# Optimization experiments

Hardware: AMD Instinct MI355X
Metric: run time of the kernel (lower is better)

Reference implementation:

```python
import jax, jax.numpy as jnp
import numpy as np

B, C, H, W = 16, 512, 32, 32

def _conv2d(x, w, b, pad):
    y = jax.lax.conv_general_dilated(
        x, w, window_strides=(1, 1), padding=[(pad, pad), (pad, pad)],
        dimension_numbers=('NCHW', 'OIHW', 'NCHW'))
    return y + b[None, :, None, None]

def setup_inputs() -> dict:
    key = jax.random.key(0)
    ks = jax.random.split(key, 10)
    s3 = 1.0 / np.sqrt(C * 9)   # torch conv2d default init scale (3x3)
    s1 = 1.0 / np.sqrt(3 * C)   # 1x1 conv over 3C input channels
    return {
        'x':  jax.random.normal(ks[0], (B, C, H, W), jnp.float32),
        'w1': jax.random.uniform(ks[1], (C, C, 3, 3), jnp.float32, -s3, s3),
        'b1': jax.random.uniform(ks[2], (C,), jnp.float32, -s3, s3),
        'w2': jax.random.uniform(ks[3], (C, C, 3, 3), jnp.float32, -s3, s3),
        'b2': jax.random.uniform(ks[4], (C,), jnp.float32, -s3, s3),
        'w3': jax.random.uniform(ks[5], (C, C, 3, 3), jnp.float32, -s3, s3),
        'b3': jax.random.uniform(ks[6], (C,), jnp.float32, -s3, s3),
        'alpha': jax.random.normal(ks[7], (), jnp.float32) * 0.1,
        'beta':  jax.random.normal(ks[8], (), jnp.float32) * 0.1,
        'wf': jax.random.uniform(ks[9], (C, 3 * C, 1, 1), jnp.float32, -s1, s1),
        'bf': jnp.zeros((C,), jnp.float32),
    }

def reference(x, w1, b1, w2, b2, w3, b3, alpha, beta, wf, bf):
    b, c, h, w = x.shape
    n = h * w
    # --- spatial attention ---
    A = _conv2d(x, w1, b1, 1).reshape(b, c, n)  # [b,C,N]
    Bm = _conv2d(x, w2, b2, 1).reshape(b, c, n)
    D = _conv2d(x, w3, b3, 1).reshape(b, c, n)
    M = jnp.einsum('bcn,bcm->bnm', A, Bm)       # A^T @ B, [b,N,N]
    M = jax.nn.softmax(M, axis=-1)
    # weighted_C = M @ D^T -> [b,N,C]; then permute to [b,C,N]
    spat = jnp.einsum('bnm,bcm->bcn', M, D).reshape(b, c, h, w)
    spat = alpha * spat
    # --- channel attention ---
    Xr = x.reshape(b, c, n)                     # [b,C,N]
    S = jnp.einsum('bcn,bdn->bcd', Xr, Xr)      # [b,C,C]
    S = jax.nn.softmax(S, axis=-1)
    # weighted = S^T @ Xr
    chan = jnp.einsum('bdc,bdn->bcn', S, Xr).reshape(b, c, h, w)
    chan = beta * chan
    # --- fuse ---
    cat = jnp.concatenate((x, spat, chan), axis=1)  # [b,3C,H,W]
    return _conv2d(cat, wf, bf, 0)
```

## Files before the change

kernel.cpp:

```cpp
#include <hip/hip_runtime.h>
#include <hip/hip_bf16.h>
#include <stdint.h>

#define B_   16
#define C_   512
#define N_   1024
#define C3   1536
#define NPAD 1156

using bf16x8 = __attribute__((ext_vector_type(8))) __bf16;
using f32x4  = __attribute__((ext_vector_type(4))) float;
typedef unsigned short ushort_t;

__device__ __forceinline__ ushort_t f2bf(float f) {
    union { float f; uint32_t u; } v; v.f = f;
    uint32_t r = v.u + 0x7FFFu + ((v.u >> 16) & 1u);
    return (ushort_t)(r >> 16);
}

typedef __attribute__((address_space(3))) void lds_void_t;
typedef const __attribute__((address_space(1))) void g_void_t;
__device__ __forceinline__ void gload16(const void* g, void* l) {
    __builtin_amdgcn_global_load_lds((g_void_t*)g, (lds_void_t*)l, 16, 0, 0);
}


__global__ void castwf_kernel(const float* __restrict__ wf,
                              ushort_t* __restrict__ Wfb,
                              ushort_t* __restrict__ zp,
                              const float* __restrict__ b1,
                              const float* __restrict__ b2,
                              const float* __restrict__ b3,
                              float* __restrict__ b_all) {
    int idx = blockIdx.x * 256 + threadIdx.x;
    if (idx < 512) zp[idx] = 0;
    if (idx < 1536) b_all[idx] = (idx < 512) ? b1[idx] : (idx < 1024) ? b2[idx - 512] : b3[idx - 1024];
    Wfb[idx] = f2bf(wf[idx]);
}

__global__ void castw3_kernel(const float* __restrict__ w1,
                              const float* __restrict__ w2,
                              const float* __restrict__ w3,
                              ushort_t* __restrict__ Wall) {
    int idx = blockIdx.x * 256 + threadIdx.x;
    int c = idx / (9 * C_ * C_);
    int r = idx - c * (9 * C_ * C_);
    int t = r / (C_ * C_);
    int rem = r - t * (C_ * C_);
    const float* w = (c == 0) ? w1 : (c == 1) ? w2 : w3;
    Wall[(size_t)t * (C3 * C_) + (size_t)c * 512 * C_ + rem] = f2bf(w[(size_t)rem * 9 + t]);
}

__global__ void castx_kernel(const float* __restrict__ x,
                             ushort_t* __restrict__ Xb,
                             ushort_t* __restrict__ cat,
                             ushort_t* __restrict__ catP) {
    __shared__ ushort_t t[32][33];
    int n0 = blockIdx.x * 32, c0 = blockIdx.y * 32, b = blockIdx.z;
    int tx = threadIdx.x & 31, ty = threadIdx.x >> 5;
    const float* xb = x + ((size_t)b * C_ + c0) * N_ + n0;
#pragma unroll
    for (int q = 0; q < 4; ++q) {
        int c = ty + q * 8;
        ushort_t h = f2bf(xb[(size_t)c * N_ + tx]);
        Xb[((size_t)b * C_ + c0 + c) * N_ + n0 + tx] = h;
        t[c][tx] = h;
    }
    __syncthreads();
#pragma unroll
    for (int q = 0; q < 4; ++q) {
        int n = ty + q * 8;
        ushort_t v = t[tx][n];
        cat[((size_t)b * N_ + n0 + n) * C3 + c0 + tx] = v;
        int prow = (n0 >> 5) * 34 + n + 35;
        catP[((size_t)b * NPAD + prow) * C_ + c0 + tx] = v;
    }
}

__global__ void transp_kernel(const ushort_t* __restrict__ Y,
                              ushort_t* __restrict__ Db) {
    __shared__ ushort_t t[32][33];
    int n0 = blockIdx.x * 32, c0 = blockIdx.y * 32, b = blockIdx.z;
    int tx = threadIdx.x & 31, ty = threadIdx.x >> 5;
#pragma unroll
    for (int q = 0; q < 4; ++q) {
        int n = ty + q * 8;
        t[n][tx] = Y[((size_t)b * N_ + n0 + n) * C3 + 1024 + c0 + tx];
    }
    __syncthreads();
#pragma unroll
    for (int q = 0; q < 4; ++q) {
        int c = ty + q * 8;
        Db[((size_t)b * C_ + c0 + c) * N_ + n0 + tx] = t[tx][c];
    }
}

__global__ void softmax_kernel(float* __restrict__ Mb) {
    int n = blockIdx.x, b = blockIdx.y;
    float* row = Mb + ((size_t)b * N_ + n) * N_;
    int tid = threadIdx.x;
    float4 v = ((const float4*)row)[tid];
    float m = fmaxf(fmaxf(v.x, v.y), fmaxf(v.z, v.w));
#pragma unroll
    for (int off = 1; off < 64; off <<= 1) m = fmaxf(m, __shfl_xor(m, off));
    __shared__ float sm[4], ss[4];
    int wid = tid >> 6, lane = tid & 63;
    if (lane == 0) sm[wid] = m;
    __syncthreads();
    m = fmaxf(fmaxf(sm[0], sm[1]), fmaxf(sm[2], sm[3]));
    float e0 = __expf(v.x - m), e1 = __expf(v.y - m);
    float e2 = __expf(v.z - m), e3 = __expf(v.w - m);
    float s = e0 + e1 + e2 + e3;
#pragma unroll
    for (int off = 1; off < 64; off <<= 1) s += __shfl_xor(s, off);
    if (lane == 0) ss[wid] = s;
    __syncthreads();
    s = ss[0] + ss[1] + ss[2] + ss[3];
    float r = 1.0f / s;
    ushort4 o;
    o.x = f2bf(e0 * r); o.y = f2bf(e1 * r); o.z = f2bf(e2 * r); o.w = f2bf(e3 * r);
    ((ushort4*)row)[tid] = o;
}

__global__ void rowstats_kernel(const float* __restrict__ S,
                                float* __restrict__ mxv, float* __restrict__ rzv) {
    int c = blockIdx.x, b = blockIdx.y;
    const float* row = S + ((size_t)b * C_ + c) * C_;
    int tid = threadIdx.x;
    float2 v = ((const float2*)row)[tid];
    float m = fmaxf(v.x, v.y);
#pragma unroll
    for (int off = 1; off < 64; off <<= 1) m = fmaxf(m, __shfl_xor(m, off));
    __shared__ float sm[4], ss[4];
    int wid = tid >> 6, lane = tid & 63;
    if (lane == 0) sm[wid] = m;
    __syncthreads();
    m = fmaxf(fmaxf(sm[0], sm[1]), fmaxf(sm[2], sm[3]));
    float e = __expf(v.x - m) + __expf(v.y - m);
#pragma unroll
    for (int off = 1; off < 64; off <<= 1) e += __shfl_xor(e, off);
    if (lane == 0) ss[wid] = e;
    __syncthreads();
    if (tid == 0) {
        e = ss[0] + ss[1] + ss[2] + ss[3];
        mxv[(size_t)b * C_ + c] = m;
        rzv[(size_t)b * C_ + c] = 1.0f / e;
    }
}

__global__ void sst_kernel(const float* __restrict__ S,
                           const float* __restrict__ mxv, const float* __restrict__ rzv,
                           ushort_t* __restrict__ Sst) {
    int idx = blockIdx.x * 256 + threadIdx.x;
    int e = idx * 4;
    int d = e & (C_ - 1);
    int b = e >> 18;
    float4 v = ((const float4*)S)[idx];
    const float* mb = mxv + ((size_t)b << 9);
    const float* rb = rzv + ((size_t)b << 9);
    ushort4 o;
    o.x = f2bf(__expf(v.x - mb[d]) * rb[d]);
    o.y = f2bf(__expf(v.y - mb[d + 1]) * rb[d + 1]);
    o.z = f2bf(__expf(v.z - mb[d + 2]) * rb[d + 2]);
    o.w = f2bf(__expf(v.w - mb[d + 3]) * rb[d + 3]);
    ((ushort4*)Sst)[idx] = o;
}

#define BM 128
#define BN 128
#define BKk 64

template <int XMODE, int OUTF32, int BIASMODE, int SCALE, int SWZ>
__global__ __launch_bounds__(256)
void gemm_bt_kernel(const ushort_t* __restrict__ Ab, int lda, long long strideA, long long tapA,
                    const ushort_t* __restrict__ Bb, int ldb, long long strideB, long long tapB,
                    void* __restrict__ Cb, int ldc, long long strideC,
                    int K, int ntaps,
                    const float* __restrict__ bias,
                    const float* __restrict__ scaleptr,
                    const ushort_t* __restrict__ zpage) {
    __shared__ short As[BM * BKk];
    __shared__ short Bs[BN * BKk];
    int tid = threadIdx.x;
    int wid = tid >> 6, lane = tid & 63;
    int wr = wid >> 1, wc = wid & 1;
    int j0 = blockIdx.x * BN, i0 = blockIdx.y * BM, b = blockIdx.z;
    const ushort_t* Abase = Ab + (size_t)b * strideA;
    const ushort_t* Bbase = Bb + (size_t)b * strideB;

    f32x4 acc[4][4] = {};

    int rs = wid * 32 + (lane >> 3);
    int kb = (lane & 7) * 8;

    for (int tap = 0; tap < ntaps; ++tap) {
        const ushort_t* At_ = Abase + (size_t)tap * tapA;
        const ushort_t* Bt_ = Bbase + (size_t)tap * tapB;
        const ushort_t* aq[4];
        const ushort_t* bq[4];
#pragma unroll
        for (int q = 0; q < 4; ++q)
            aq[q] = At_ + (size_t)(i0 + rs + q * 8) * lda + kb;
#pragma unroll
        for (int q = 0; q < 4; ++q)
            bq[q] = Bt_ + (size_t)(j0 + rs + q * 8) * ldb + kb;

        for (int kk = 0; kk < K; kk += BKk) {
            __syncthreads();
#pragma unroll
            for (int q = 0; q < 4; ++q) {
                gload16(aq[q], &As[(wid * 32 + q * 8) * BKk]);
                aq[q] += BKk;
                gload16(bq[q], &Bs[(wid * 32 + q * 8) * BKk]);
                bq[q] += BKk;
            }
            __syncthreads();
#pragma unroll
            for (int kc = 0; kc < BKk; kc += 32) {
                bf16x8 af[4], bfr[4];
#pragma unroll
                for (int m = 0; m < 4; ++m)
                    af[m] = *(const bf16x8*)&As[(wr * 64 + m * 16 + (lane & 15)) * BKk + kc + (lane >> 4) * 8];
#pragma unroll
                for (int nb = 0; nb < 4; ++nb)
                    bfr[nb] = *(const bf16x8*)&Bs[(wc * 64 + nb * 16 + (lane & 15)) * BKk + kc + (lane >> 4) * 8];
#pragma unroll
                for (int m = 0; m < 4; ++m)
#pragma unroll
                    for (int nb = 0; nb < 4; ++nb)
                        acc[m][nb] = __builtin_amdgcn_mfma_f32_16x16x32_bf16(af[m], bfr[nb], acc[m][nb], 0, 0, 0);
            }
        }
    }

    float scale = SCALE ? *scaleptr : 1.0f;
#pragma unroll
    for (int m = 0; m < 4; ++m) {
#pragma unroll
        for (int nb = 0; nb < 4; ++nb) {
            int i = i0 + wr * 64 + m * 16 + (lane >> 4) * 4;
            int j = j0 + wc * 64 + nb * 16 + (lane & 15);
#pragma unroll
            for (int r = 0; r < 4; ++r) {
                float v = acc[m][nb][r];
                if (BIASMODE == 1) v += bias[i + r];
                if (BIASMODE == 2) v += bias[j];
                if (SCALE) v *= scale;
                if (OUTF32)
                    ((float*)Cb)[(size_t)b * strideC + (size_t)(i + r) * ldc + j] = v;
                else
                    ((ushort_t*)Cb)[(size_t)b * strideC + (size_t)(i + r) * ldc + j] = f2bf(v);
            }
        }
    }
}

#define R3BM 256
#define R3BN 128
#define R3BK 64

template <int XMODE, int OUTF32, int BIASMODE, int SCALE>
__global__ __launch_bounds__(512, 2)
void gemm_r3_kernel(const ushort_t* __restrict__ Ab, int lda, long long strideA, long long tapA,
                    const ushort_t* __restrict__ Bb, int ldb, long long strideB, long long tapB,
                    void* __restrict__ Cb, int ldc, long long strideC,
                    int K, int ntaps,
                    const float* __restrict__ bias,
                    const float* __restrict__ scaleptr,
                    const ushort_t* __restrict__ zpage) {
    __shared__ short As[3][R3BM * R3BK];
    __shared__ short Bs[3][R3BN * R3BK];
    int tid = threadIdx.x;
    int wid = tid >> 6, lane = tid & 63;
    int wr = wid >> 1, wc = wid & 1;
    int j0 = blockIdx.x * R3BN, i0 = blockIdx.y * R3BM, b = blockIdx.z;
    int kpt = K >> 6;
    int nt = ntaps * kpt;

    f32x4 acc[4][4] = {};

    int sr = tid >> 3;
    int klds = (tid & 7) * 8;
    int sbase = wid * 512;

    int aoff[4][2], boff[4][2];
#pragma unroll
    for (int m = 0; m < 4; ++m) {
        int row = wr * 64 + m * 16 + (lane & 15);
        int sw = (row & 7) << 3;
#pragma unroll
        for (int h = 0; h < 2; ++h)
            aoff[m][h] = row * R3BK + ((h * 32 + (lane >> 4) * 8) ^ sw);
    }
#pragma unroll
    for (int nb = 0; nb < 4; ++nb) {
        int row = wc * 64 + nb * 16 + (lane & 15);
        int sw = (row & 7) << 3;
#pragma unroll
        for (int h = 0; h < 2; ++h)
            boff[nb][h] = row * R3BK + ((h * 32 + (lane >> 4) * 8) ^ sw);
    }

    const ushort_t* pa[4];
    const ushort_t* pb[2];
#pragma unroll
    for (int s = 0; s < 4; ++s) {
        int r = sr + s * 64;
        int ks = klds ^ ((r & 7) << 3);
        if (XMODE == 1) {
            int li = (i0 & (N_ - 1)) + r;
            int pr = (li >> 5) * 34 + (li & 31) + 35;
            pa[s] = Ab + ((size_t)(i0 >> 10) * NPAD + pr) * lda + ks;
        } else {
            pa[s] = Ab + (size_t)b * strideA + (size_t)(i0 + r) * lda + ks;
        }
    }
#pragma unroll
    for (int s = 0; s < 2; ++s) {
        int r = sr + s * 64;
        int ks = klds ^ ((r & 7) << 3);
        pb[s] = Bb + (size_t)b * strideB + (size_t)(j0 + r) * ldb + ks;
    }

    int s_tap = 0, s_kk = 0;
    auto STAGE = [&](int slot) {
        long long uA, uB;
        if (XMODE == 1) {
            int dh = s_tap / 3 - 1, dw = s_tap - (s_tap / 3) * 3 - 1;
            uA = (long long)(dh * 34 + dw) * lda + s_kk * R3BK;
        } else {
            uA = (long long)s_tap * tapA + (long long)s_kk * R3BK;
        }
        uB = (long long)s_tap * tapB + (long long)s_kk * R3BK;
#pragma unroll
        for (int s = 0; s < 4; ++s)
            gload16(pa[s] + uA, &As[slot][sbase + s * 4096]);
#pragma unroll
        for (int s = 0; s < 2; ++s)
            gload16(pb[s] + uB, &Bs[slot][sbase + s * 4096]);
        if (++s_tap == ntaps) { s_tap = 0; ++s_kk; }
    };

    STAGE(0);
    STAGE(1);

    for (int t = 0; t < nt; ++t) {
        int slot = t - (t / 3) * 3;
        if (t + 1 < nt) asm volatile("s_waitcnt vmcnt(6)" ::: "memory");
        else            asm volatile("s_waitcnt vmcnt(0)" ::: "memory");
        __builtin_amdgcn_s_barrier();
        __builtin_amdgcn_sched_barrier(0);

        const short* Aslot = &As[slot][0];
        const short* Bslot = &Bs[slot][0];
        bf16x8 af[4][2], bfr[4][2];
#pragma unroll
        for (int h = 0; h < 2; ++h) {
#pragma unroll
            for (int m = 0; m < 4; ++m)
                af[m][h] = *(const bf16x8*)&Aslot[aoff[m][h]];
#pragma unroll
            for (int nb = 0; nb < 4; ++nb)
                bfr[nb][h] = *(const bf16x8*)&Bslot[boff[nb][h]];
        }

        if (t + 2 < nt) STAGE((t + 2) - ((t + 2) / 3) * 3);

        asm volatile("s_waitcnt lgkmcnt(8)" ::: "memory");
        __builtin_amdgcn_sched_barrier(0);
        __builtin_amdgcn_s_setprio(1);
#pragma unroll
        for (int m = 0; m < 4; ++m)
#pragma unroll
            for (int nb = 0; nb < 4; ++nb)
                acc[m][nb] = __builtin_amdgcn_mfma_f32_16x16x32_bf16(af[m][0], bfr[nb][0], acc[m][nb], 0, 0, 0);
        asm volatile("s_waitcnt lgkmcnt(0)" ::: "memory");
        __builtin_amdgcn_sched_barrier(0);
#pragma unroll
        for (int m = 0; m < 4; ++m)
#pragma unroll
            for (int nb = 0; nb < 4; ++nb)
                acc[m][nb] = __builtin_amdgcn_mfma_f32_16x16x32_bf16(af[m][1], bfr[nb][1], acc[m][nb], 0, 0, 0);
        __builtin_amdgcn_s_setprio(0);
    }

    float scale = SCALE ? *scaleptr : 1.0f;
#pragma unroll
    for (int m = 0; m < 4; ++m) {
#pragma unroll
        for (int nb = 0; nb < 4; ++nb) {
            int i = i0 + wr * 64 + m * 16 + (lane >> 4) * 4;
            int j = j0 + wc * 64 + nb * 16 + (lane & 15);
#pragma unroll
            for (int r = 0; r < 4; ++r) {
                float v = acc[m][nb][r];
                if (BIASMODE == 1) v += bias[i + r];
                if (BIASMODE == 2) v += bias[j];
                if (SCALE) v *= scale;
                if (OUTF32)
                    ((float*)Cb)[(size_t)b * strideC + (size_t)(i + r) * ldc + j] = v;
                else
                    ((ushort_t*)Cb)[(size_t)b * strideC + (size_t)(i + r) * ldc + j] = f2bf(v);
            }
        }
    }
}

constexpr size_t OFF_ZP   = 0;
constexpr size_t OFF_BALL = 1024;
constexpr size_t OFF_WFB  = OFF_BALL + 6144;
constexpr size_t OFF_CAT  = OFF_WFB + (size_t)C_ * C3 * 2;
constexpr size_t OFF_Y    = OFF_CAT + (size_t)B_ * N_ * C3 * 2;
constexpr size_t OFF_DB   = OFF_Y + (size_t)B_ * N_ * C3 * 2;
constexpr size_t OFF_SR   = OFF_DB + (size_t)B_ * C_ * N_ * 2;
constexpr size_t OFF_SST  = OFF_SR + (size_t)B_ * C_ * C_ * 4;
constexpr size_t OFF_MX   = OFF_SST + (size_t)B_ * C_ * C_ * 2;
constexpr size_t OFF_RZ   = OFF_MX + (size_t)B_ * C_ * 4;
constexpr size_t OFF_U    = OFF_RZ + (size_t)B_ * C_ * 4;
constexpr size_t WALL_SZ  = (size_t)9 * C3 * C_ * 2;
constexpr size_t XB_SZ    = (size_t)B_ * C_ * N_ * 2;
constexpr size_t CATP_SZ  = (size_t)B_ * NPAD * C_ * 2;
constexpr size_t OFF_WALL = OFF_U;
constexpr size_t OFF_XB   = OFF_U + WALL_SZ;
constexpr size_t OFF_CATP = OFF_XB + XB_SZ;
constexpr size_t OFF_M    = OFF_U;
constexpr size_t EXT_A    = OFF_CATP + CATP_SZ;
constexpr size_t EXT_B    = OFF_M + (size_t)B_ * N_ * N_ * 4;
constexpr size_t WS_NEED  = EXT_A > EXT_B ? EXT_A : EXT_B;

extern "C" void kernel_launch(void* const* d_in, const int* in_sizes, int n_in,
                              void* d_out, int out_size, void* d_ws, size_t ws_size,
                              hipStream_t stream) {
    const float* x   = (const float*)d_in[0];
    const float* w1  = (const float*)d_in[1];
    const float* b1  = (const float*)d_in[2];
    const float* w2  = (const float*)d_in[3];
    const float* b2  = (const float*)d_in[4];
    const float* w3  = (const float*)d_in[5];
    const float* b3  = (const float*)d_in[6];
    const float* alpha = (const float*)d_in[7];
    const float* beta  = (const float*)d_in[8];
    const float* wf  = (const float*)d_in[9];
    const float* bfv = (const float*)d_in[10];
    float* out = (float*)d_out;
    char* ws = (char*)d_ws;
    if (ws_size < WS_NEED) return;

    ushort_t* zp   = (ushort_t*)(ws + OFF_ZP);
    float*    ball = (float*)(ws + OFF_BALL);
    ushort_t* Wfb  = (ushort_t*)(ws + OFF_WFB);
    ushort_t* cat  = (ushort_t*)(ws + OFF_CAT);
    ushort_t* Y    = (ushort_t*)(ws + OFF_Y);
    ushort_t* Db   = (ushort_t*)(ws + OFF_DB);
    float*    Sr   = (float*)(ws + OFF_SR);
    ushort_t* Sst  = (ushort_t*)(ws + OFF_SST);
    float*    mxv  = (float*)(ws + OFF_MX);
    float*    rzv  = (float*)(ws + OFF_RZ);
    ushort_t* Wall = (ushort_t*)(ws + OFF_WALL);
    ushort_t* Xb   = (ushort_t*)(ws + OFF_XB);
    ushort_t* catP = (ushort_t*)(ws + OFF_CATP);
    float*    Mb   = (float*)(ws + OFF_M);

    hipMemsetAsync(catP, 0, CATP_SZ, stream);

    castwf_kernel<<<(C_ * C3) / 256, 256, 0, stream>>>(wf, Wfb, zp, b1, b2, b3, ball);
    castw3_kernel<<<(3 * 9 * C_ * C_) / 256, 256, 0, stream>>>(w1, w2, w3, Wall);
    castx_kernel<<<dim3(N_ / 32, C_ / 32, B_), 256, 0, stream>>>(x, Xb, cat, catP);

    gemm_r3_kernel<1, 0, 2, 0><<<dim3(12, 64, 1), 512, 0, stream>>>(
        catP, C_, 0, 0,
        Wall, C_, 0, (long long)C3 * C_,
        Y, C3, 0,
        C_, 9, ball, nullptr, zp);
    transp_kernel<<<dim3(N_ / 32, C_ / 32, B_), 256, 0, stream>>>(Y, Db);
    gemm_bt_kernel<0, 1, 0, 0, 0><<<dim3(4, 4, B_), 256, 0, stream>>>(
        Xb, N_, (long long)C_ * N_, 0,
        Xb, N_, (long long)C_ * N_, 0,
        Sr, C_, (long long)C_ * C_,
        N_, 1, nullptr, nullptr, zp);
    rowstats_kernel<<<dim3(C_, B_), 256, 0, stream>>>(Sr, mxv, rzv);
    sst_kernel<<<(B_ * C_ * C_ / 4) / 256, 256, 0, stream>>>(Sr, mxv, rzv, Sst);
    gemm_r3_kernel<0, 1, 0, 0><<<dim3(8, 4, B_), 512, 0, stream>>>(
        Y, C3, (long long)N_ * C3, 0,
        Y + 512, C3, (long long)N_ * C3, 0,
        Mb, N_, (long long)N_ * N_,
        C_, 1, nullptr, nullptr, zp);
    softmax_kernel<<<dim3(N_, B_), 256, 0, stream>>>(Mb);
    gemm_r3_kernel<0, 0, 0, 1><<<dim3(4, 4, B_), 512, 0, stream>>>(
        (const ushort_t*)Mb, 2048, (long long)N_ * 2048, 0,
        Db, N_, (long long)C_ * N_, 0,
        cat + 512, C3, (long long)N_ * C3,
        N_, 1, nullptr, alpha, zp);
    gemm_r3_kernel<0, 0, 0, 1><<<dim3(4, 4, B_), 512, 0, stream>>>(
        cat, C3, (long long)N_ * C3, 0,
        Sst, C_, (long long)C_ * C_, 0,
        cat + 1024, C3, (long long)N_ * C3,
        C_, 1, nullptr, beta, zp);
    gemm_r3_kernel<0, 1, 1, 0><<<dim3(8, 2, B_), 512, 0, stream>>>(
        Wfb, C3, 0, 0,
        cat, C3, (long long)N_ * C3, 0,
        out, N_, (long long)C_ * N_,
        C3, 1, bfv, nullptr, zp);
}
```

Baseline: 434.9 us.

## Add 256-thread triple-buffered GEMM variant with larger per-wave tiles for 3x3 conv

Adds a new implicit-GEMM kernel for the fused QKV 3x3 convolution. It uses 4 waves of 256 threads instead of 8, with each wave computing a 128x64 output sub-tile (8x4 MFMA accumulators), and triple-buffers LDS through async global-to-LDS loads. The aim is more MFMA work per LDS fragment load and deeper overlap of loads with compute. In exchange, register pressure roughly doubles and fewer waves are available to hide latency.

```diff
diff --git a/kernel.cpp b/kernel.cpp
--- a/kernel.cpp
+++ b/kernel.cpp
@@ -390,6 +390,156 @@
 #pragma unroll
         for (int nb = 0; nb < 4; ++nb) {
             int i = i0 + wr * 64 + m * 16 + (lane >> 4) * 4;
+            int j = j0 + wc * 64 + nb * 16 + (lane & 15);
+#pragma unroll
+            for (int r = 0; r < 4; ++r) {
+                float v = acc[m][nb][r];
+                if (BIASMODE == 1) v += bias[i + r];
+                if (BIASMODE == 2) v += bias[j];
+                if (SCALE) v *= scale;
+                if (OUTF32)
+                    ((float*)Cb)[(size_t)b * strideC + (size_t)(i + r) * ldc + j] = v;
+                else
+                    ((ushort_t*)Cb)[(size_t)b * strideC + (size_t)(i + r) * ldc + j] = f2bf(v);
+            }
+        }
+    }
+}
+
+#define RFBM 256
+#define RFBN 128
+#define RFBK 64
+
+template <int XMODE, int OUTF32, int BIASMODE, int SCALE>
+__global__ __launch_bounds__(256, 1)
+void gemm_r3f_kernel(const ushort_t* __restrict__ Ab, int lda, long long strideA, long long tapA,
+                     const ushort_t* __restrict__ Bb, int ldb, long long strideB, long long tapB,
+                     void* __restrict__ Cb, int ldc, long long strideC,
+                     int K, int ntaps,
+                     const float* __restrict__ bias,
+                     const float* __restrict__ scaleptr) {
+    __shared__ short As[3][RFBM * RFBK];
+    __shared__ short Bs[3][RFBN * RFBK];
+    int tid = threadIdx.x;
+    int wid = tid >> 6, lane = tid & 63;
+    int wr = wid >> 1, wc = wid & 1;
+    int j0 = blockIdx.x * RFBN, i0 = blockIdx.y * RFBM, b = blockIdx.z;
+    int kpt = K >> 6;
+    int nt = ntaps * kpt;
+
+    f32x4 acc[8][4] = {};
+
+    int sr = tid >> 3;
+    int klds = (tid & 7) * 8;
+    int sbase = wid * 512;
+
+    int aoff[8][2], boff[4][2];
+#pragma unroll
+    for (int m = 0; m < 8; ++m) {
+        int row = wr * 128 + m * 16 + (lane & 15);
+        int sw = (row & 7) << 3;
+#pragma unroll
+        for (int h = 0; h < 2; ++h)
+            aoff[m][h] = row * RFBK + ((h * 32 + (lane >> 4) * 8) ^ sw);
+    }
+#pragma unroll
+    for (int nb = 0; nb < 4; ++nb) {
+        int row = wc * 64 + nb * 16 + (lane & 15);
+        int sw = (row & 7) << 3;
+#pragma unroll
+        for (int h = 0; h < 2; ++h)
+            boff[nb][h] = row * RFBK + ((h * 32 + (lane >> 4) * 8) ^ sw);
+    }
+
+    const ushort_t* pa[8];
+    const ushort_t* pb[4];
+#pragma unroll
+    for (int s = 0; s < 8; ++s) {
+        int r = sr + s * 32;
+        int ks = klds ^ ((r & 7) << 3);
+        if (XMODE == 1) {
+            int li = (i0 & (N_ - 1)) + r;
+            int pr = (li >> 5) * 34 + (li & 31) + 35;
+            pa[s] = Ab + ((size_t)(i0 >> 10) * NPAD + pr) * lda + ks;
+        } else {
+            pa[s] = Ab + (size_t)b * strideA + (size_t)(i0 + r) * lda + ks;
+        }
+    }
+#pragma unroll
+    for (int s = 0; s < 4; ++s) {
+        int r = sr + s * 32;
+        int ks = klds ^ ((r & 7) << 3);
+        pb[s] = Bb + (size_t)b * strideB + (size_t)(j0 + r) * ldb + ks;
+    }
+
+    int s_tap = 0, s_kk = 0;
+    auto STAGE = [&](int slot) {
+        long long uA, uB;
+        if (XMODE == 1) {
+            int dh = s_tap / 3 - 1, dw = s_tap - (s_tap / 3) * 3 - 1;
+            uA = (long long)(dh * 34 + dw) * lda + s_kk * RFBK;
+        } else {
+            uA = (long long)s_tap * tapA + (long long)s_kk * RFBK;
+        }
+        uB = (long long)s_tap * tapB + (long long)s_kk * RFBK;
+#pragma unroll
+        for (int s = 0; s < 8; ++s)
+            gload16(pa[s] + uA, &As[slot][sbase + s * 2048]);
+#pragma unroll
+        for (int s = 0; s < 4; ++s)
+            gload16(pb[s] + uB, &Bs[slot][sbase + s * 2048]);
+        if (++s_tap == ntaps) { s_tap = 0; ++s_kk; }
+    };
+
+    STAGE(0);
+    STAGE(1);
+
+    for (int t = 0; t < nt; ++t) {
+        int slot = t - (t / 3) * 3;
+        if (t + 1 < nt) asm volatile("s_waitcnt vmcnt(12)" ::: "memory");
+        else            asm volatile("s_waitcnt vmcnt(0)" ::: "memory");
+        __builtin_amdgcn_s_barrier();
+        __builtin_amdgcn_sched_barrier(0);
+
+        const short* Aslot = &As[slot][0];
+        const short* Bslot = &Bs[slot][0];
+        bf16x8 af[8][2], bfr[4][2];
+#pragma unroll
+        for (int h = 0; h < 2; ++h) {
+#pragma unroll
+            for (int m = 0; m < 8; ++m)
+                af[m][h] = *(const bf16x8*)&Aslot[aoff[m][h]];
+#pragma unroll
+            for (int nb = 0; nb < 4; ++nb)
+                bfr[nb][h] = *(const bf16x8*)&Bslot[boff[nb][h]];
+        }
+
+        if (t + 2 < nt) STAGE((t + 2) - ((t + 2) / 3) * 3);
+
+        asm volatile("s_waitcnt lgkmcnt(12)" ::: "memory");
+        __builtin_amdgcn_sched_barrier(0);
+        __builtin_amdgcn_s_setprio(1);
+#pragma unroll
+        for (int m = 0; m < 8; ++m)
+#pragma unroll
+            for (int nb = 0; nb < 4; ++nb)
+                acc[m][nb] = __builtin_amdgcn_mfma_f32_16x16x32_bf16(af[m][0], bfr[nb][0], acc[m][nb], 0, 0, 0);
+        asm volatile("s_waitcnt lgkmcnt(0)" ::: "memory");
+        __builtin_amdgcn_sched_barrier(0);
+#pragma unroll
+        for (int m = 0; m < 8; ++m)
+#pragma unroll
+            for (int nb = 0; nb < 4; ++nb)
+                acc[m][nb] = __builtin_amdgcn_mfma_f32_16x16x32_bf16(af[m][1], bfr[nb][1], acc[m][nb], 0, 0, 0);
+        __builtin_amdgcn_s_setprio(0);
+    }
+
+    float scale = SCALE ? *scaleptr : 1.0f;
+#pragma unroll
+    for (int m = 0; m < 8; ++m) {
+#pragma unroll
+        for (int nb = 0; nb < 4; ++nb) {
+            int i = i0 + wr * 128 + m * 16 + (lane >> 4) * 4;
             int j = j0 + wc * 64 + nb * 16 + (lane & 15);
 #pragma unroll
             for (int r = 0; r < 4; ++r) {
@@ -467,11 +617,11 @@
     castw3_kernel<<<(3 * 9 * C_ * C_) / 256, 256, 0, stream>>>(w1, w2, w3, Wall);
     castx_kernel<<<dim3(N_ / 32, C_ / 32, B_), 256, 0, stream>>>(x, Xb, cat, catP);
 
-    gemm_r3_kernel<1, 0, 2, 0><<<dim3(12, 64, 1), 512, 0, stream>>>(
+    gemm_r3f_kernel<1, 0, 2, 0><<<dim3(12, 64, 1), 256, 0, stream>>>(
         catP, C_, 0, 0,
         Wall, C_, 0, (long long)C3 * C_,
         Y, C3, 0,
-        C_, 9, ball, nullptr, zp);
+        C_, 9, ball, nullptr);
     transp_kernel<<<dim3(N_ / 32, C_ / 32, B_), 256, 0, stream>>>(Y, Db);
     gemm_bt_kernel<0, 1, 0, 0, 0><<<dim3(4, 4, B_), 256, 0, stream>>>(
         Xb, N_, (long long)C_ * N_, 0,
```

Result: slower. 462.5 us (+6.4%).
